# Kernel tuning notes

Measured on AMD Instinct MI355X. Metric: run time of the kernel, lower is better.

Reference implementation:

```python
import jax, jax.numpy as jnp
import numpy as np

HEADS = 4
DIM_HEAD = 32
SCALE = DIM_HEAD ** -0.5


def setup_inputs() -> dict:
    key = jax.random.key(0)
    ks = jax.random.split(key, 7)
    b, c, h, w = 2, 256, 64, 64
    time_dim = 512
    hidden = HEADS * DIM_HEAD  # 128
    return {
        "x": jax.random.normal(ks[0], (b, c, h, w), jnp.float32),
        "time_emb": jax.random.normal(ks[1], (b, time_dim), jnp.float32),
        "w_mlp": jax.random.normal(ks[2], (2 * c, time_dim), jnp.float32) * 0.02,
        "b_mlp": jax.random.normal(ks[3], (2 * c,), jnp.float32) * 0.02,
        "w_qkv": jax.random.normal(ks[4], (3 * hidden, c), jnp.float32) * 0.05,
        "w_out": jax.random.normal(ks[5], (c, hidden), jnp.float32) * 0.05,
        "b_out": jax.random.normal(ks[6], (c,), jnp.float32) * 0.02,
    }


def reference(x, time_emb, w_mlp, b_mlp, w_qkv, w_out, b_out):
    b, c, h, w = x.shape
    n = h * w
    # FiLM conditioning: SiLU -> Linear -> chunk into (scale, shift)
    t = jax.nn.silu(time_emb) @ w_mlp.T + b_mlp            # [b, 2c]
    scale, shift = jnp.split(t, 2, axis=1)                  # [b, c] each
    x = x * (scale + 1.0)[:, :, None, None] + shift[:, :, None, None]
    # 1x1 conv QKV projection (no bias)
    qkv = jnp.einsum('oc,bchw->bohw', w_qkv, x)             # [b, 3*hidden, h, w]
    q, k, v = jnp.split(qkv, 3, axis=1)                     # [b, hidden, h, w]
    def to_heads(t):
        return t.reshape(b, HEADS, DIM_HEAD, n)             # b h d (x y)
    q, k, v = to_heads(q) * SCALE, to_heads(k), to_heads(v)
    sim = jnp.einsum('bhdi,bhdj->bhij', q, k)               # [b, h, n, n]
    attn = jax.nn.softmax(sim, axis=-1)
    out = jnp.einsum('bhij,bhdj->bhid', attn, v)            # [b, h, n, d]
    # b h (x y) d -> b (h d) x y
    out = out.transpose(0, 1, 3, 2).reshape(b, HEADS * DIM_HEAD, h, w)
    return jnp.einsum('oc,bchw->bohw', w_out, out) + b_out[None, :, None, None]
```

## Files before the change

kernel.cpp:

```cpp
#include <hip/hip_runtime.h>


typedef __bf16 bf16x8 __attribute__((ext_vector_type(8)));
typedef float  f32x16 __attribute__((ext_vector_type(16)));
typedef unsigned uint2v __attribute__((ext_vector_type(2)));

#define MFMA(a, b, c) __builtin_amdgcn_mfma_f32_32x32x16_bf16((a), (b), (c), 0, 0, 0)
#define PLSWAP(a, b) __builtin_amdgcn_permlane32_swap((a), (b), false, false)

static constexpr float kLOG2E = 1.4426950408889634f;
static constexpr float kSCALE = 0.17677669529663687f;

__device__ __forceinline__ unsigned short bf16r(float x) {
  union { float f; unsigned u; } v; v.f = x;
  return (unsigned short)((v.u + 0x7FFFu + ((v.u >> 16) & 1u)) >> 16);
}
__device__ __forceinline__ float fast_silu(float x) {
  return x / (1.0f + __builtin_amdgcn_exp2f(-x * kLOG2E));
}
__device__ __forceinline__ f32x16 zero16() {
  f32x16 z;
#pragma unroll
  for (int i = 0; i < 16; ++i) z[i] = 0.0f;
  return z;
}
__device__ __forceinline__ bf16x8 ld_frag(const unsigned short* p) {
  return *reinterpret_cast<const bf16x8*>(p);
}

__global__ __launch_bounds__(256) void prep(const float* __restrict__ x,
                                            unsigned short* __restrict__ xT,
                                            const float* __restrict__ te,
                                            const float* __restrict__ w_mlp,
                                            const float* __restrict__ b_mlp,
                                            float* __restrict__ fparams) {
  __shared__ unsigned short lds[64][66];
  int bid = blockIdx.x;
  if (bid < 32) {
    int g = bid * 256 + threadIdx.x;
    int pair = g >> 3, ks = g & 7;
    int b = pair >> 9, o = pair & 511;
    const float4* w4 = (const float4*)(w_mlp + (size_t)o * 512 + ks * 64);
    const float4* t4 = (const float4*)(te + (size_t)b * 512 + ks * 64);
    float s = 0.0f;
#pragma unroll 4
    for (int k = 0; k < 16; ++k) {
      float4 wv = w4[k];
      float4 tv = t4[k];
      s += wv.x * fast_silu(tv.x) + wv.y * fast_silu(tv.y) +
           wv.z * fast_silu(tv.z) + wv.w * fast_silu(tv.w);
    }
    s += __shfl_xor(s, 1, 64);
    s += __shfl_xor(s, 2, 64);
    s += __shfl_xor(s, 4, 64);
    if (ks == 0) {
      float t_val = s + b_mlp[o];
      fparams[b * 512 + o] = (o < 256) ? (t_val + 1.0f) : t_val;
    }
    return;
  }
  int bid2 = bid - 32;
  int p0 = (bid2 & 63) * 64;
  int c0 = ((bid2 >> 6) & 3) * 64;
  int b  = bid2 >> 8;
  int t = threadIdx.x;
  int pl = t & 63, cw = t >> 6;
  const float* xb = x + ((size_t)b * 256 + c0) * 4096 + p0;
#pragma unroll
  for (int r = 0; r < 16; ++r) {
    int cl = cw + r * 4;
    lds[pl][cl] = bf16r(xb[(size_t)cl * 4096 + pl]);
  }
  __syncthreads();
  unsigned short* out = xT + ((size_t)b * 4096 + p0) * 256 + c0;
#pragma unroll
  for (int rep = 0; rep < 2; ++rep) {
    int ch = t + rep * 256;
    int pr = ch >> 3, cc = (ch & 7) * 8;
    union { unsigned short u[8]; uint4 v; } pk;
#pragma unroll
    for (int i = 0; i < 8; ++i) pk.u[i] = lds[pr][cc + i];
    *(uint4*)(out + (size_t)pr * 256 + cc) = pk.v;
  }
}

__global__ __launch_bounds__(256) void film2(const float* __restrict__ w_qkv,
                                             const float* __restrict__ fparams,
                                             const float* __restrict__ w_out,
                                             unsigned short* __restrict__ Aeff,
                                             float* __restrict__ qb,
                                             unsigned short* __restrict__ WoBf) {
  int tid = blockIdx.x * 256 + threadIdx.x;
  if (tid < 24576) {
    int row = tid >> 5, cs = tid & 31;
    int b = row / 384, o = row % 384;
    float qs = (o < 128) ? (kSCALE * kLOG2E) : 1.0f;
    const float4* wr  = (const float4*)(w_qkv + (size_t)o * 256);
    const float4* sc4 = (const float4*)(fparams + b * 512);
    const float4* sh4 = (const float4*)(fparams + b * 512 + 256);
    unsigned short* arow = Aeff + ((size_t)b * 384 + o) * 256;
    float acc = 0.0f;
#pragma unroll
    for (int j = 0; j < 2; ++j) {
      int c4 = cs * 2 + j;
      float4 wv = wr[c4], scv = sc4[c4], shv = sh4[c4];
      acc += wv.x * shv.x + wv.y * shv.y + wv.z * shv.z + wv.w * shv.w;
      union { unsigned short u[4]; unsigned long long q; } pk;
      pk.u[0] = bf16r(wv.x * scv.x * qs);
      pk.u[1] = bf16r(wv.y * scv.y * qs);
      pk.u[2] = bf16r(wv.z * scv.z * qs);
      pk.u[3] = bf16r(wv.w * scv.w * qs);
      *(unsigned long long*)(arow + c4 * 4) = pk.q;
    }
    acc += __shfl_xor(acc, 1, 64);
    acc += __shfl_xor(acc, 2, 64);
    acc += __shfl_xor(acc, 4, 64);
    acc += __shfl_xor(acc, 8, 64);
    acc += __shfl_xor(acc, 16, 64);
    if (cs == 0) qb[b * 384 + o] = acc * qs;
  } else {
    int t = tid - 24576;
    const float4* src = (const float4*)(w_out + (size_t)t * 64);
    unsigned short* dst = WoBf + (size_t)t * 64;
#pragma unroll 4
    for (int i = 0; i < 16; ++i) {
      float4 v = src[i];
      union { unsigned short u[4]; unsigned long long q; } pk;
      pk.u[0] = bf16r(v.x); pk.u[1] = bf16r(v.y);
      pk.u[2] = bf16r(v.z); pk.u[3] = bf16r(v.w);
      *(unsigned long long*)(dst + i * 4) = pk.q;
    }
  }
}

__global__ __launch_bounds__(64) void qkv_gemm(const unsigned short* __restrict__ Aeff,
                                               const float* __restrict__ qb,
                                               const unsigned short* __restrict__ xT,
                                               unsigned short* __restrict__ Qb,
                                               unsigned short* __restrict__ Kb,
                                               unsigned short* __restrict__ Vt) {
  int bid = blockIdx.x;
  int o_blk = bid % 12;
  int rest = bid / 12;
  int b = rest & 1, p_blk = rest >> 1;
  int l = threadIdx.x, col = l & 31, hi = l >> 5;

  const unsigned short* Ab = Aeff + ((size_t)b * 384 + o_blk * 32) * 256;
  const unsigned short* Bb = xT + ((size_t)b * 4096 + p_blk * 32) * 256;

  f32x16 acc = zero16();
#pragma unroll
  for (int kc = 0; kc < 256; kc += 16) {
    bf16x8 a0 = ld_frag(Ab + (size_t)col * 256 + kc + hi * 8);
    bf16x8 b0 = ld_frag(Bb + (size_t)col * 256 + kc + hi * 8);
    acc = MFMA(a0, b0, acc);
  }

  int obase = o_blk * 32;
  int sec = obase >> 7;
  int head = (obase & 127) >> 5;
  size_t bh = (size_t)b * 4 + head;
  int p = p_blk * 32 + col;
  if (sec < 2) {
    unsigned short* dst = (sec == 0 ? Qb : Kb) + (bh * 4096 + p) * 32;
#pragma unroll
    for (int g = 0; g < 4; ++g) {
      int dbase = 8 * g + 4 * hi;
      union { unsigned short u[4]; unsigned long long q; } pk;
#pragma unroll
      for (int r = 0; r < 4; ++r)
        pk.u[r] = bf16r(acc[4 * g + r] + qb[b * 384 + obase + dbase + r]);
      *(unsigned long long*)(dst + dbase) = pk.q;
    }
  } else {
    unsigned short* dst = Vt + bh * 32 * 4096;
#pragma unroll
    for (int reg = 0; reg < 16; ++reg) {
      int d = (reg & 3) + 8 * (reg >> 2) + 4 * hi;
      dst[(size_t)d * 4096 + p] = bf16r(acc[reg] + qb[b * 384 + obase + d]);
    }
  }
}

__device__ __forceinline__ void softmax_pv(f32x16 S, bf16x8 va0, bf16x8 va1,
                                           f32x16& O, float& lsum) {
#pragma unroll
  for (int i = 0; i < 16; ++i) S[i] = __builtin_amdgcn_exp2f(S[i]);
  float s0 = (S[0] + S[1]) + (S[2] + S[3]);
  float s1 = (S[4] + S[5]) + (S[6] + S[7]);
  float s2 = (S[8] + S[9]) + (S[10] + S[11]);
  float s3 = (S[12] + S[13]) + (S[14] + S[15]);
  lsum += (s0 + s1) + (s2 + s3);
  union { __bf16 h[16]; unsigned u[8]; } pu;
#pragma unroll
  for (int i = 0; i < 16; ++i) pu.h[i] = (__bf16)S[i];
  uint2v r0 = PLSWAP(pu.u[0], pu.u[2]);
  uint2v r1 = PLSWAP(pu.u[1], pu.u[3]);
  uint2v r2 = PLSWAP(pu.u[4], pu.u[6]);
  uint2v r3 = PLSWAP(pu.u[5], pu.u[7]);
  union { unsigned u[4]; bf16x8 v; } B0, B1;
  B0.u[0] = r0[0]; B0.u[1] = r1[0]; B0.u[2] = r0[1]; B0.u[3] = r1[1];
  B1.u[0] = r2[0]; B1.u[1] = r3[0]; B1.u[2] = r2[1]; B1.u[3] = r3[1];
  O = MFMA(va0, B0.v, O);
  O = MFMA(va1, B1.v, O);
}

__global__ __launch_bounds__(256, 4) void attn(const unsigned short* __restrict__ Qb,
                                               const unsigned short* __restrict__ Kb,
                                               const unsigned short* __restrict__ Vt,
                                               unsigned short* __restrict__ Ob) {
  __shared__ float Olds[4][16][64];
  __shared__ float llds[4][64];

  int bid = blockIdx.x;
  int bh = bid >> 7;
  int q0 = (bid & 127) * 32;
  int w = threadIdx.x >> 6;
  int l = threadIdx.x & 63, col = l & 31, hi = l >> 5;

  const unsigned short* Qp = Qb + ((size_t)bh * 4096 + q0) * 32;
  bf16x8 qf0 = ld_frag(Qp + col * 32 + hi * 8);
  bf16x8 qf1 = ld_frag(Qp + col * 32 + 16 + hi * 8);

  const unsigned short* kp =
      Kb + (size_t)bh * 131072 + (size_t)(w * 1024 + col) * 32 + hi * 8;
  const unsigned short* vp =
      Vt + (size_t)bh * 131072 + (size_t)col * 4096 + w * 1024 + hi * 8;

  const f32x16 zc = zero16();
  f32x16 O = zero16();
  float lsum = 0.0f;

  bf16x8 ka0 = ld_frag(kp),      ka1 = ld_frag(kp + 16);
  bf16x8 va0 = ld_frag(vp),      va1 = ld_frag(vp + 16);
  kp += 1024; vp += 32;
  bf16x8 kb0 = ld_frag(kp),      kb1 = ld_frag(kp + 16);
  bf16x8 vb0 = ld_frag(vp),      vb1 = ld_frag(vp + 16);

  for (int it = 0; it < 16; ++it) {
    f32x16 S = MFMA(ka0, qf0, zc);
    S = MFMA(ka1, qf1, S);
    kp += 1024; vp += 32;
    ka0 = ld_frag(kp); ka1 = ld_frag(kp + 16);
    bf16x8 pva0 = va0, pva1 = va1;
    va0 = ld_frag(vp); va1 = ld_frag(vp + 16);
    softmax_pv(S, pva0, pva1, O, lsum);

    f32x16 S2 = MFMA(kb0, qf0, zc);
    S2 = MFMA(kb1, qf1, S2);
    kp += 1024; vp += 32;
    kb0 = ld_frag(kp); kb1 = ld_frag(kp + 16);
    bf16x8 pvb0 = vb0, pvb1 = vb1;
    vb0 = ld_frag(vp); vb1 = ld_frag(vp + 16);
    softmax_pv(S2, pvb0, pvb1, O, lsum);
  }

  uint2v lr = PLSWAP(__float_as_uint(lsum), __float_as_uint(lsum));
  float lt = __uint_as_float(lr[0]) + __uint_as_float(lr[1]);

#pragma unroll
  for (int i = 0; i < 16; ++i) Olds[w][i][l] = O[i];
  llds[w][l] = lt;
  __syncthreads();

  float L = (llds[0][l] + llds[1][l]) + (llds[2][l] + llds[3][l]);
  float inv = 1.0f / L;

  union { unsigned short u[4]; unsigned long long q; } pk4;
#pragma unroll
  for (int r = 0; r < 4; ++r) {
    int reg = 4 * w + r;
    float v = Olds[0][reg][l] + Olds[1][reg][l] + Olds[2][reg][l] + Olds[3][reg][l];
    pk4.u[r] = bf16r(v * inv);
  }
  unsigned short* dst = Ob + ((size_t)bh * 4096 + q0 + col) * 32 + 8 * w + 4 * hi;
  *(unsigned long long*)dst = pk4.q;
}

__global__ __launch_bounds__(64) void out_gemm(const unsigned short* __restrict__ Wo,
                                               const unsigned short* __restrict__ Ob,
                                               const float* __restrict__ b_out,
                                               float* __restrict__ out) {
  int bid = blockIdx.x;
  int o_blk = bid & 7;
  int rest = bid >> 3;
  int b = rest & 1, p_blk = rest >> 1;
  int l = threadIdx.x, col = l & 31, hi = l >> 5;

  const unsigned short* Ab = Wo + (size_t)(o_blk * 32) * 128;
  f32x16 acc = zero16();
#pragma unroll
  for (int kc = 0; kc < 128; kc += 16) {
    int head = kc >> 5;
    int doff = (kc & 16) + hi * 8;
    const unsigned short* Bb =
        Ob + (((size_t)b * 4 + head) * 4096 + p_blk * 32) * 32 + doff;
    bf16x8 a0 = ld_frag(Ab + (size_t)col * 128 + kc + hi * 8);
    bf16x8 b0 = ld_frag(Bb + (size_t)col * 32);
    acc = MFMA(a0, b0, acc);
  }
  int p = p_blk * 32 + col;
#pragma unroll
  for (int reg = 0; reg < 16; ++reg) {
    int o = o_blk * 32 + (reg & 3) + 8 * (reg >> 2) + 4 * hi;
    out[((size_t)b * 256 + o) * 4096 + p] = acc[reg] + b_out[o];
  }
}

extern "C" void kernel_launch(void* const* d_in, const int* in_sizes, int n_in,
                              void* d_out, int out_size, void* d_ws, size_t ws_size,
                              hipStream_t stream) {
  const float* x     = (const float*)d_in[0];
  const float* te    = (const float*)d_in[1];
  const float* w_mlp = (const float*)d_in[2];
  const float* b_mlp = (const float*)d_in[3];
  const float* w_qkv = (const float*)d_in[4];
  const float* w_out = (const float*)d_in[5];
  const float* b_out = (const float*)d_in[6];

  char* ws = (char*)d_ws;
  float*          fparams = (float*)(ws + 0);
  float*          qb      = (float*)(ws + 4096);
  unsigned short* Aeff    = (unsigned short*)(ws + 8192);
  unsigned short* WoBf    = (unsigned short*)(ws + 401408);
  unsigned short* xT      = (unsigned short*)(ws + 466944);
  unsigned short* Qb      = (unsigned short*)(ws + 4661248);
  unsigned short* Kb      = (unsigned short*)(ws + 6758400);
  unsigned short* Vt      = (unsigned short*)(ws + 8855552);
  unsigned short* Ob      = (unsigned short*)(ws + 10952704);
  float* out = (float*)d_out;

  hipLaunchKernelGGL(prep, dim3(544), dim3(256), 0, stream, x, xT, te, w_mlp,
                     b_mlp, fparams);
  hipLaunchKernelGGL(film2, dim3(98), dim3(256), 0, stream, w_qkv, fparams, w_out,
                     Aeff, qb, WoBf);
  hipLaunchKernelGGL(qkv_gemm, dim3(3072), dim3(64), 0, stream, Aeff, qb, xT, Qb, Kb, Vt);
  hipLaunchKernelGGL(attn, dim3(1024), dim3(256), 0, stream, Qb, Kb, Vt, Ob);
  hipLaunchKernelGGL(out_gemm, dim3(2048), dim3(64), 0, stream, WoBf, Ob, b_out, out);
}
```

Before: 149.4 us.

## Process two query/pixel tiles per block to reuse K/V and weight fragments

Each attention block now handles 64 queries instead of 32, so every loaded K and V fragment feeds two score/PV chains. The explicit double-buffered prefetch is dropped in favour of a simple per-iteration load. The QKV and output GEMMs likewise compute two 32-pixel tiles per wave and reuse the A fragment, halving grid sizes. The cost is more registers and LDS per block (occupancy hint lowered to 3), fewer blocks in flight, and less explicit latency hiding in the attention loop.

```diff
diff --git a/kernel.cpp b/kernel.cpp
--- a/kernel.cpp
+++ b/kernel.cpp
@@ -146,38 +146,45 @@
   int l = threadIdx.x, col = l & 31, hi = l >> 5;
 
   const unsigned short* Ab = Aeff + ((size_t)b * 384 + o_blk * 32) * 256;
-  const unsigned short* Bb = xT + ((size_t)b * 4096 + p_blk * 32) * 256;
-
-  f32x16 acc = zero16();
+  const unsigned short* Bb = xT + ((size_t)b * 4096 + p_blk * 64) * 256;
+
+  f32x16 acc0 = zero16(), acc1 = zero16();
 #pragma unroll
   for (int kc = 0; kc < 256; kc += 16) {
     bf16x8 a0 = ld_frag(Ab + (size_t)col * 256 + kc + hi * 8);
     bf16x8 b0 = ld_frag(Bb + (size_t)col * 256 + kc + hi * 8);
-    acc = MFMA(a0, b0, acc);
+    bf16x8 b1 = ld_frag(Bb + (size_t)(col + 32) * 256 + kc + hi * 8);
+    acc0 = MFMA(a0, b0, acc0);
+    acc1 = MFMA(a0, b1, acc1);
   }
 
   int obase = o_blk * 32;
   int sec = obase >> 7;
   int head = (obase & 127) >> 5;
   size_t bh = (size_t)b * 4 + head;
-  int p = p_blk * 32 + col;
-  if (sec < 2) {
-    unsigned short* dst = (sec == 0 ? Qb : Kb) + (bh * 4096 + p) * 32;
-#pragma unroll
-    for (int g = 0; g < 4; ++g) {
-      int dbase = 8 * g + 4 * hi;
-      union { unsigned short u[4]; unsigned long long q; } pk;
-#pragma unroll
-      for (int r = 0; r < 4; ++r)
-        pk.u[r] = bf16r(acc[4 * g + r] + qb[b * 384 + obase + dbase + r]);
-      *(unsigned long long*)(dst + dbase) = pk.q;
-    }
-  } else {
-    unsigned short* dst = Vt + bh * 32 * 4096;
-#pragma unroll
-    for (int reg = 0; reg < 16; ++reg) {
-      int d = (reg & 3) + 8 * (reg >> 2) + 4 * hi;
-      dst[(size_t)d * 4096 + p] = bf16r(acc[reg] + qb[b * 384 + obase + d]);
+  f32x16 accs[2] = {acc0, acc1};
+#pragma unroll
+  for (int pt = 0; pt < 2; ++pt) {
+    int p = p_blk * 64 + pt * 32 + col;
+    f32x16 acc = accs[pt];
+    if (sec < 2) {
+      unsigned short* dst = (sec == 0 ? Qb : Kb) + (bh * 4096 + p) * 32;
+#pragma unroll
+      for (int g = 0; g < 4; ++g) {
+        int dbase = 8 * g + 4 * hi;
+        union { unsigned short u[4]; unsigned long long q; } pk;
+#pragma unroll
+        for (int r = 0; r < 4; ++r)
+          pk.u[r] = bf16r(acc[4 * g + r] + qb[b * 384 + obase + dbase + r]);
+        *(unsigned long long*)(dst + dbase) = pk.q;
+      }
+    } else {
+      unsigned short* dst = Vt + bh * 32 * 4096;
+#pragma unroll
+      for (int reg = 0; reg < 16; ++reg) {
+        int d = (reg & 3) + 8 * (reg >> 2) + 4 * hi;
+        dst[(size_t)d * 4096 + p] = bf16r(acc[reg] + qb[b * 384 + obase + d]);
+      }
     }
   }
 }
@@ -205,22 +212,24 @@
   O = MFMA(va1, B1.v, O);
 }
 
-__global__ __launch_bounds__(256, 4) void attn(const unsigned short* __restrict__ Qb,
+__global__ __launch_bounds__(256, 3) void attn(const unsigned short* __restrict__ Qb,
                                                const unsigned short* __restrict__ Kb,
                                                const unsigned short* __restrict__ Vt,
                                                unsigned short* __restrict__ Ob) {
-  __shared__ float Olds[4][16][64];
-  __shared__ float llds[4][64];
+  __shared__ float Olds[4][2][16][64];
+  __shared__ float llds[4][2][64];
 
   int bid = blockIdx.x;
-  int bh = bid >> 7;
-  int q0 = (bid & 127) * 32;
+  int bh = bid >> 6;
+  int q0 = (bid & 63) * 64;
   int w = threadIdx.x >> 6;
   int l = threadIdx.x & 63, col = l & 31, hi = l >> 5;
 
   const unsigned short* Qp = Qb + ((size_t)bh * 4096 + q0) * 32;
   bf16x8 qf0 = ld_frag(Qp + col * 32 + hi * 8);
   bf16x8 qf1 = ld_frag(Qp + col * 32 + 16 + hi * 8);
+  bf16x8 qg0 = ld_frag(Qp + (col + 32) * 32 + hi * 8);
+  bf16x8 qg1 = ld_frag(Qp + (col + 32) * 32 + 16 + hi * 8);
 
   const unsigned short* kp =
       Kb + (size_t)bh * 131072 + (size_t)(w * 1024 + col) * 32 + hi * 8;
@@ -228,53 +237,55 @@
       Vt + (size_t)bh * 131072 + (size_t)col * 4096 + w * 1024 + hi * 8;
 
   const f32x16 zc = zero16();
-  f32x16 O = zero16();
-  float lsum = 0.0f;
-
-  bf16x8 ka0 = ld_frag(kp),      ka1 = ld_frag(kp + 16);
-  bf16x8 va0 = ld_frag(vp),      va1 = ld_frag(vp + 16);
-  kp += 1024; vp += 32;
-  bf16x8 kb0 = ld_frag(kp),      kb1 = ld_frag(kp + 16);
-  bf16x8 vb0 = ld_frag(vp),      vb1 = ld_frag(vp + 16);
-
-  for (int it = 0; it < 16; ++it) {
-    f32x16 S = MFMA(ka0, qf0, zc);
-    S = MFMA(ka1, qf1, S);
+  f32x16 Oa = zero16(), Obb = zero16();
+  float lsuma = 0.0f, lsumb = 0.0f;
+
+  for (int it = 0; it < 32; ++it) {
+    bf16x8 ka0 = ld_frag(kp);
+    bf16x8 ka1 = ld_frag(kp + 16);
+    bf16x8 va0 = ld_frag(vp);
+    bf16x8 va1 = ld_frag(vp + 16);
     kp += 1024; vp += 32;
-    ka0 = ld_frag(kp); ka1 = ld_frag(kp + 16);
-    bf16x8 pva0 = va0, pva1 = va1;
-    va0 = ld_frag(vp); va1 = ld_frag(vp + 16);
-    softmax_pv(S, pva0, pva1, O, lsum);
-
-    f32x16 S2 = MFMA(kb0, qf0, zc);
-    S2 = MFMA(kb1, qf1, S2);
-    kp += 1024; vp += 32;
-    kb0 = ld_frag(kp); kb1 = ld_frag(kp + 16);
-    bf16x8 pvb0 = vb0, pvb1 = vb1;
-    vb0 = ld_frag(vp); vb1 = ld_frag(vp + 16);
-    softmax_pv(S2, pvb0, pvb1, O, lsum);
-  }
-
-  uint2v lr = PLSWAP(__float_as_uint(lsum), __float_as_uint(lsum));
-  float lt = __uint_as_float(lr[0]) + __uint_as_float(lr[1]);
-
-#pragma unroll
-  for (int i = 0; i < 16; ++i) Olds[w][i][l] = O[i];
-  llds[w][l] = lt;
+
+    f32x16 Sa = MFMA(ka0, qf0, zc);
+    Sa = MFMA(ka1, qf1, Sa);
+    f32x16 Sb = MFMA(ka0, qg0, zc);
+    Sb = MFMA(ka1, qg1, Sb);
+
+    softmax_pv(Sa, va0, va1, Oa, lsuma);
+    softmax_pv(Sb, va0, va1, Obb, lsumb);
+  }
+
+  uint2v lra = PLSWAP(__float_as_uint(lsuma), __float_as_uint(lsuma));
+  uint2v lrb = PLSWAP(__float_as_uint(lsumb), __float_as_uint(lsumb));
+  float lta = __uint_as_float(lra[0]) + __uint_as_float(lra[1]);
+  float ltb = __uint_as_float(lrb[0]) + __uint_as_float(lrb[1]);
+
+#pragma unroll
+  for (int i = 0; i < 16; ++i) {
+    Olds[w][0][i][l] = Oa[i];
+    Olds[w][1][i][l] = Obb[i];
+  }
+  llds[w][0][l] = lta;
+  llds[w][1][l] = ltb;
   __syncthreads();
 
-  float L = (llds[0][l] + llds[1][l]) + (llds[2][l] + llds[3][l]);
-  float inv = 1.0f / L;
-
-  union { unsigned short u[4]; unsigned long long q; } pk4;
-#pragma unroll
-  for (int r = 0; r < 4; ++r) {
-    int reg = 4 * w + r;
-    float v = Olds[0][reg][l] + Olds[1][reg][l] + Olds[2][reg][l] + Olds[3][reg][l];
-    pk4.u[r] = bf16r(v * inv);
-  }
-  unsigned short* dst = Ob + ((size_t)bh * 4096 + q0 + col) * 32 + 8 * w + 4 * hi;
-  *(unsigned long long*)dst = pk4.q;
+#pragma unroll
+  for (int h = 0; h < 2; ++h) {
+    float L = (llds[0][h][l] + llds[1][h][l]) + (llds[2][h][l] + llds[3][h][l]);
+    float inv = 1.0f / L;
+    union { unsigned short u[4]; unsigned long long q; } pk4;
+#pragma unroll
+    for (int r = 0; r < 4; ++r) {
+      int reg = 4 * w + r;
+      float v = (Olds[0][h][reg][l] + Olds[1][h][reg][l]) +
+                (Olds[2][h][reg][l] + Olds[3][h][reg][l]);
+      pk4.u[r] = bf16r(v * inv);
+    }
+    unsigned short* dst =
+        Ob + ((size_t)bh * 4096 + q0 + h * 32 + col) * 32 + 8 * w + 4 * hi;
+    *(unsigned long long*)dst = pk4.q;
+  }
 }
 
 __global__ __launch_bounds__(64) void out_gemm(const unsigned short* __restrict__ Wo,
@@ -288,22 +299,29 @@
   int l = threadIdx.x, col = l & 31, hi = l >> 5;
 
   const unsigned short* Ab = Wo + (size_t)(o_blk * 32) * 128;
-  f32x16 acc = zero16();
+  f32x16 acc0 = zero16(), acc1 = zero16();
 #pragma unroll
   for (int kc = 0; kc < 128; kc += 16) {
     int head = kc >> 5;
     int doff = (kc & 16) + hi * 8;
     const unsigned short* Bb =
-        Ob + (((size_t)b * 4 + head) * 4096 + p_blk * 32) * 32 + doff;
+        Ob + (((size_t)b * 4 + head) * 4096 + p_blk * 64) * 32 + doff;
     bf16x8 a0 = ld_frag(Ab + (size_t)col * 128 + kc + hi * 8);
     bf16x8 b0 = ld_frag(Bb + (size_t)col * 32);
-    acc = MFMA(a0, b0, acc);
-  }
-  int p = p_blk * 32 + col;
-#pragma unroll
-  for (int reg = 0; reg < 16; ++reg) {
-    int o = o_blk * 32 + (reg & 3) + 8 * (reg >> 2) + 4 * hi;
-    out[((size_t)b * 256 + o) * 4096 + p] = acc[reg] + b_out[o];
+    bf16x8 b1 = ld_frag(Bb + (size_t)(col + 32) * 32);
+    acc0 = MFMA(a0, b0, acc0);
+    acc1 = MFMA(a0, b1, acc1);
+  }
+  f32x16 accs[2] = {acc0, acc1};
+#pragma unroll
+  for (int pt = 0; pt < 2; ++pt) {
+    int p = p_blk * 64 + pt * 32 + col;
+    f32x16 acc = accs[pt];
+#pragma unroll
+    for (int reg = 0; reg < 16; ++reg) {
+      int o = o_blk * 32 + (reg & 3) + 8 * (reg >> 2) + 4 * hi;
+      out[((size_t)b * 256 + o) * 4096 + p] = acc[reg] + b_out[o];
+    }
   }
 }
 
@@ -334,7 +352,7 @@
                      b_mlp, fparams);
   hipLaunchKernelGGL(film2, dim3(98), dim3(256), 0, stream, w_qkv, fparams, w_out,
                      Aeff, qb, WoBf);
-  hipLaunchKernelGGL(qkv_gemm, dim3(3072), dim3(64), 0, stream, Aeff, qb, xT, Qb, Kb, Vt);
-  hipLaunchKernelGGL(attn, dim3(1024), dim3(256), 0, stream, Qb, Kb, Vt, Ob);
-  hipLaunchKernelGGL(out_gemm, dim3(2048), dim3(64), 0, stream, WoBf, Ob, b_out, out);
-}
+  hipLaunchKernelGGL(qkv_gemm, dim3(1536), dim3(64), 0, stream, Aeff, qb, xT, Qb, Kb, Vt);
+  hipLaunchKernelGGL(attn, dim3(512), dim3(256), 0, stream, Qb, Kb, Vt, Ob);
+  hipLaunchKernelGGL(out_gemm, dim3(1024), dim3(64), 0, stream, WoBf, Ob, b_out, out);
+}
```

New measurement: 133.2 us. 1.12x faster.
